# Performance work log

Hardware: AMD Instinct MI355X
Metric: run time of the kernel (lower is better)

## Reference

```python
import jax, jax.numpy as jnp
import numpy as np

N, NF, D, GH, E, B = 4096, 128, 64, 64, 32768, 32
NG, STEPS = 3, 3  # n_gcn, set2set processing steps


def setup_inputs() -> dict:
    key = jax.random.key(0)
    ks = iter(jax.random.split(key, 64))
    nrm = lambda shape: jax.random.normal(next(ks), shape, dtype=jnp.float32) * 0.05
    inp = {
        'x': jax.random.normal(next(ks), (N, NF), dtype=jnp.float32),
        'edge_attr': jax.random.uniform(next(ks), (E,), dtype=jnp.float32),
        'edge_idx': jax.random.randint(next(ks), (2, E), 0, N),
        'batch_map': jnp.sort(jax.random.randint(next(ks), (N,), 0, B)),
        # pre-GC MLP: NF->D, D->D, D->D (ReLU each)
        'pre_W0': nrm((NF, D)), 'pre_b0': nrm((D,)),
        'pre_W1': nrm((D, D)), 'pre_b1': nrm((D,)),
        'pre_W2': nrm((D, D)), 'pre_b2': nrm((D,)),
        # NNConv edge nets (stacked over NG layers): 1->GH->D*D
        'enn_W1': nrm((NG, 1, GH)), 'enn_b1': nrm((NG, GH)),
        'enn_W2': nrm((NG, GH, D * D)), 'enn_b2': nrm((NG, D * D)),
        'root_W': nrm((NG, D, D)), 'conv_b': nrm((NG, D)),
        # GRU(D, D) per layer, gate order r,z,n (torch), stored transposed for x@W
        'gru_Wih': nrm((NG, D, 3 * D)), 'gru_Whh': nrm((NG, D, 3 * D)),
        'gru_bih': nrm((NG, 3 * D)), 'gru_bhh': nrm((NG, 3 * D)),
        # Set2Set LSTM: input 2D -> hidden D, gate order i,f,g,o (torch)
        's2s_Wih': nrm((2 * D, 4 * D)), 's2s_Whh': nrm((D, 4 * D)),
        's2s_bih': nrm((4 * D,)), 's2s_bhh': nrm((4 * D,)),
        # post-GC MLP: 2D->D, D->D, D->D (ReLU each), then D->1
        'post_W0': nrm((2 * D, D)), 'post_b0': nrm((D,)),
        'post_W1': nrm((D, D)), 'post_b1': nrm((D,)),
        'post_W2': nrm((D, D)), 'post_b2': nrm((D,)),
        'post_W3': nrm((D, 1)), 'post_b3': nrm((1,)),
    }
    return inp


def _forward(x, edge_attr, pre_W0, pre_b0, pre_W1, pre_b1, pre_W2, pre_b2,
             enn_W1, enn_b1, enn_W2, enn_b2, root_W, conv_b,
             gru_Wih, gru_Whh, gru_bih, gru_bhh,
             s2s_Wih, s2s_Whh, s2s_bih, s2s_bhh,
             post_W0, post_b0, post_W1, post_b1, post_W2, post_b2,
             post_W3, post_b3, edge_idx, batch_map):
    relu, sig = jax.nn.relu, jax.nn.sigmoid
    # pre-GC layers
    out = relu(x @ pre_W0 + pre_b0)
    out = relu(out @ pre_W1 + pre_b1)
    out = relu(out @ pre_W2 + pre_b2)  # [N, D]

    src, dst = edge_idx[0], edge_idx[1]
    deg = jax.ops.segment_sum(jnp.ones((E,), out.dtype), dst, num_segments=N)
    deg = jnp.maximum(deg, 1.0)
    ea = edge_attr[:, None]  # view(-1, 1)

    for l in range(NG):
        h = out
        # NNConv: per-edge weight matrix from edge MLP
        We = relu(ea @ enn_W1[l] + enn_b1[l])              # [E, GH]
        We = (We @ enn_W2[l] + enn_b2[l]).reshape(E, D, D)  # [E, D, D]
        msg = jnp.einsum('ei,eio->eo', out[src], We)        # [E, D]
        agg = jax.ops.segment_sum(msg, dst, num_segments=N) / deg[:, None]
        conv = relu(agg + out @ root_W[l] + conv_b[l])
        # single-step GRU update (torch gate order r, z, n)
        gi = conv @ gru_Wih[l] + gru_bih[l]
        gh = h @ gru_Whh[l] + gru_bhh[l]
        i_r, i_z, i_n = jnp.split(gi, 3, axis=-1)
        h_r, h_z, h_n = jnp.split(gh, 3, axis=-1)
        r = sig(i_r + h_r)
        z = sig(i_z + h_z)
        n = jnp.tanh(i_n + r * h_n)
        out = (1.0 - z) * n + z * h

    # Set2Set pooling (early)
    q_star = jnp.zeros((B, 2 * D), out.dtype)
    hh = jnp.zeros((B, D), out.dtype)
    cc = jnp.zeros((B, D), out.dtype)
    for _ in range(STEPS):
        gates = q_star @ s2s_Wih + s2s_bih + hh @ s2s_Whh + s2s_bhh
        gi_, gf, gg, go = jnp.split(gates, 4, axis=-1)
        cc = sig(gf) * cc + sig(gi_) * jnp.tanh(gg)
        hh = sig(go) * jnp.tanh(cc)
        q = hh
        e = jnp.sum(out * q[batch_map], axis=-1)                    # [N]
        m = jax.ops.segment_max(e, batch_map, num_segments=B)
        a = jnp.exp(e - m[batch_map])
        den = jax.ops.segment_sum(a, batch_map, num_segments=B)
        a = a / den[batch_map]
        r_read = jax.ops.segment_sum(a[:, None] * out, batch_map, num_segments=B)
        q_star = jnp.concatenate([q, r_read], axis=-1)              # [B, 2D]

    # post-GC layers
    y = relu(q_star @ post_W0 + post_b0)
    y = relu(y @ post_W1 + post_b1)
    y = relu(y @ post_W2 + post_b2)
    y = y @ post_W3 + post_b3  # [B, 1]
    return y


def reference(x, edge_attr, edge_idx, batch_map, pre_W0, pre_b0, pre_W1, pre_b1,
              pre_W2, pre_b2, enn_W1, enn_b1, enn_W2, enn_b2, root_W, conv_b,
              gru_Wih, gru_Whh, gru_bih, gru_bhh, s2s_Wih, s2s_Whh, s2s_bih,
              s2s_bhh, post_W0, post_b0, post_W1, post_b1, post_W2, post_b2,
              post_W3, post_b3):
    return _forward(x, edge_attr, pre_W0, pre_b0, pre_W1, pre_b1, pre_W2, pre_b2,
                    enn_W1, enn_b1, enn_W2, enn_b2, root_W, conv_b,
                    gru_Wih, gru_Whh, gru_bih, gru_bhh,
                    s2s_Wih, s2s_Whh, s2s_bih, s2s_bhh,
                    post_W0, post_b0, post_W1, post_b1, post_W2, post_b2,
                    post_W3, post_b3, edge_idx, batch_map)
```

## Files before the change

### kernel.cpp

```cpp
#include <hip/hip_runtime.h>
#include <hip/hip_bf16.h>
#include <string.h>

#define NN   4096
#define NE   32768
#define NB   32
#define BKT  64
#define MSG_CHUNK 8

typedef __attribute__((ext_vector_type(8))) short short8;
typedef __attribute__((ext_vector_type(4))) float f4;

__device__ __forceinline__ float sigf(float x) { return 1.0f / (1.0f + __expf(-x)); }
__device__ __forceinline__ short f2bf(float f) {
    __hip_bfloat16 h = __float2bfloat16(f);
    short s;
    memcpy(&s, &h, sizeof(short));
    return s;
}

__global__ __launch_bounds__(256) void k_setup(const float* __restrict__ x,
        const float* __restrict__ W0, const float* __restrict__ b0,
        const float* __restrict__ W1, const float* __restrict__ b1,
        const float* __restrict__ W2, const float* __restrict__ b2,
        const float* __restrict__ enn_W2, __hip_bfloat16* __restrict__ W2F,
        float* __restrict__ out, float* __restrict__ agg,
        int* cnt_src, int* cnt_dst, int* bstart, int* bend) {
    int bid = blockIdx.x, t = threadIdx.x;
    if (bid < 32) {
        int i = bid * 256 + t;
        if (i < NN) cnt_src[i] = 0;
        else cnt_dst[i - NN] = 0;
        if (i < NB) { bstart[i] = 0x7FFFFFFF; bend[i] = 0; }
    } else if (bid < 224) {
        __shared__ __hip_bfloat16 tile[4096];
        size_t base = (size_t)(bid - 32) * 4096;
        for (int i = t; i < 4096; i += 256) {
            int k = i >> 6, o = i & 63;
            int pos = ((o >> 4) << 10) | ((k >> 5) << 9) | (((k >> 3) & 3) << 7)
                    | ((o & 15) << 3) | (k & 7);
            tile[pos] = __float2bfloat16(enn_W2[base + i]);
        }
        __syncthreads();
        for (int i = t; i < 4096; i += 256) W2F[base + i] = tile[i];
    } else {
        __shared__ float xr[4][128], ha[4][64], hb[4][64];
        int w = t >> 6, j = t & 63;
        int n = (bid - 224) * 4 + w;
        xr[w][j] = x[(size_t)n * 128 + j];
        xr[w][64 + j] = x[(size_t)n * 128 + 64 + j];
        agg[(size_t)n * 64 + j] = 0.f;
        float s = b0[j];
        #pragma unroll 8
        for (int k = 0; k < 128; ++k) s = fmaf(xr[w][k], W0[k * 64 + j], s);
        ha[w][j] = fmaxf(s, 0.f);
        s = b1[j];
        #pragma unroll 8
        for (int k = 0; k < 64; ++k) s = fmaf(ha[w][k], W1[k * 64 + j], s);
        hb[w][j] = fmaxf(s, 0.f);
        s = b2[j];
        #pragma unroll 8
        for (int k = 0; k < 64; ++k) s = fmaf(hb[w][k], W2[k * 64 + j], s);
        out[(size_t)n * 64 + j] = fmaxf(s, 0.f);
    }
}

__global__ __launch_bounds__(256) void k_bucket(const int* __restrict__ eidx,
        const float* __restrict__ ea, const int* __restrict__ bm,
        int* cnt_src, int* cnt_dst, int* csr_dst, float* csr_ea,
        int* bstart, int* bend) {
    int e = blockIdx.x * 256 + threadIdx.x;
    if (e < NE) {
        int s = eidx[e];
        int d = eidx[NE + e];
        int slot = atomicAdd(&cnt_src[s], 1);
        if (slot < BKT) {
            csr_dst[s * BKT + slot] = d;
            csr_ea[s * BKT + slot] = ea[e];
        }
        atomicAdd(&cnt_dst[d], 1);
    }
    if (e < NN) {
        int b = bm[e];
        atomicMin(&bstart[b], e);
        atomicMax(&bend[b], e + 1);
    }
}

__global__ __launch_bounds__(256, 2) void k_fused(const float* __restrict__ out,
        const __hip_bfloat16* __restrict__ W2F_l, const float* __restrict__ b2l,
        const float* __restrict__ W1l, const float* __restrict__ b1l,
        const int* __restrict__ cnt_src, const int* __restrict__ csr_dst,
        const float* __restrict__ csr_ea, float* __restrict__ agg) {
    __shared__ __hip_bfloat16 Pt[8 * 4096];
    __shared__ float outs[8][68];
    __shared__ float wlds[4][MSG_CHUNK][64];
    int t = threadIdx.x, wave = t >> 6, lane = t & 63;
    int laneM = lane & 15, quad = lane >> 4;
    int n0 = blockIdx.x * 8;
    for (int i = t; i < 512; i += 256) outs[i >> 6][i & 63] = out[(size_t)n0 * 64 + i];
    __syncthreads();
    short8 a0, a1;
    {
        const float* ar = &outs[laneM & 7][quad * 8];
        #pragma unroll
        for (int j = 0; j < 8; ++j) a0[j] = f2bf(ar[j]);
        const float* ar2 = &outs[laneM & 7][32 + quad * 8];
        #pragma unroll
        for (int j = 0; j < 8; ++j) a1[j] = f2bf(ar2[j]);
    }
    float btr[2] = {0.f, 0.f};
    for (int k = 0; k < 64; ++k) {
        float bv = b2l[k * 64 + lane];
        #pragma unroll
        for (int u = 0; u < 2; ++u) btr[u] = fmaf(outs[wave * 2 + u][k], bv, btr[u]);
    }
    #pragma unroll 2
    for (int gp = 0; gp < 8; ++gp) {
        int gA = wave * 16 + gp * 2;
        const __hip_bfloat16* BgA = W2F_l + (size_t)gA * 4096;
        const __hip_bfloat16* BgB = BgA + 4096;
        int c = gA >> 3;
        int p = (gA >> 1) & 3;
        char* wb = (char*)Pt + (quad << 15) + (c << 10) + (laneM << 4)
                 + (((p ^ quad) & 3) << 2);
        #pragma unroll
        for (int sub = 0; sub < 4; ++sub) {
            short8 bA0 = *(const short8*)(BgA + sub * 1024 + lane * 8);
            short8 bA1 = *(const short8*)(BgA + sub * 1024 + 512 + lane * 8);
            short8 bB0 = *(const short8*)(BgB + sub * 1024 + lane * 8);
            short8 bB1 = *(const short8*)(BgB + sub * 1024 + 512 + lane * 8);
            f4 accA = {0.f, 0.f, 0.f, 0.f}, accB = {0.f, 0.f, 0.f, 0.f};
            accA = __builtin_amdgcn_mfma_f32_16x16x32_bf16(a0, bA0, accA, 0, 0, 0);
            accA = __builtin_amdgcn_mfma_f32_16x16x32_bf16(a1, bA1, accA, 0, 0, 0);
            accB = __builtin_amdgcn_mfma_f32_16x16x32_bf16(a0, bB0, accB, 0, 0, 0);
            accB = __builtin_amdgcn_mfma_f32_16x16x32_bf16(a1, bB1, accB, 0, 0, 0);
            if (quad < 2) {
                char* wbs = wb + (sub << 8);
                #pragma unroll
                for (int r = 0; r < 4; ++r) {
                    unsigned pk = (unsigned)(unsigned short)f2bf(accA[r])
                                | ((unsigned)(unsigned short)f2bf(accB[r]) << 16);
                    *(unsigned*)(wbs + (r << 13)) = pk;
                }
            }
        }
    }
    __syncthreads();
    float w1v = W1l[lane], b1v = b1l[lane];
    for (int u = 0; u < 2; ++u) {
        int nloc = wave * 2 + u;
        int n = n0 + nloc;
        int deg = cnt_src[n];
        if (deg > BKT) deg = BKT;
        if (deg <= 0) continue;
        int wq = nloc >> 2;
        float preg[64];
        const char* Pn = (const char*)Pt + (nloc << 13);
        #pragma unroll
        for (int c = 0; c < 8; ++c) {
            uint4 vv = *(const uint4*)(Pn + (c << 10) + (lane << 4));
            unsigned d0 = vv.x, d1 = vv.y, d2 = vv.z, d3 = vv.w;
            if (wq & 1) { unsigned tt = d0; d0 = d1; d1 = tt; tt = d2; d2 = d3; d3 = tt; }
            union { unsigned u2; float f; } cv;
            cv.u2 = d0 << 16;          preg[c * 8 + 0] = cv.f;
            cv.u2 = d0 & 0xFFFF0000u;  preg[c * 8 + 1] = cv.f;
            cv.u2 = d1 << 16;          preg[c * 8 + 2] = cv.f;
            cv.u2 = d1 & 0xFFFF0000u;  preg[c * 8 + 3] = cv.f;
            cv.u2 = d2 << 16;          preg[c * 8 + 4] = cv.f;
            cv.u2 = d2 & 0xFFFF0000u;  preg[c * 8 + 5] = cv.f;
            cv.u2 = d3 << 16;          preg[c * 8 + 6] = cv.f;
            cv.u2 = d3 & 0xFFFF0000u;  preg[c * 8 + 7] = cv.f;
        }
        float bt = btr[u];
        const int* bdst = csr_dst + n * BKT;
        const float* bea = csr_ea + n * BKT;
        for (int c0 = 0; c0 < deg; c0 += MSG_CHUNK) {
            int cc = deg - c0;
            if (cc > MSG_CHUNK) cc = MSG_CHUNK;
            int dl = 0; float el = 0.f;
            if (lane < cc) { dl = bdst[c0 + lane]; el = bea[c0 + lane]; }
            for (int si = 0; si < cc; ++si) {
                float eav = __shfl(el, si, 64);
                wlds[wave][si][lane] = fmaxf(fmaf(eav, w1v, b1v), 0.f);
            }
            for (int i = 0; i < cc; ++i) {
                int dst = __shfl(dl, i, 64);
                const float* wr = wlds[wave][i];
                float acc0 = bt, acc1 = 0.f, acc2 = 0.f, acc3 = 0.f;
                #pragma unroll
                for (int g = 0; g < 64; g += 16) {
                    float4 w0 = *(const float4*)(wr + g);
                    float4 w1 = *(const float4*)(wr + g + 4);
                    float4 w2 = *(const float4*)(wr + g + 8);
                    float4 w3 = *(const float4*)(wr + g + 12);
                    acc0 = fmaf(w0.x, preg[g], acc0);
                    acc0 = fmaf(w0.y, preg[g + 1], acc0);
                    acc0 = fmaf(w0.z, preg[g + 2], acc0);
                    acc0 = fmaf(w0.w, preg[g + 3], acc0);
                    acc1 = fmaf(w1.x, preg[g + 4], acc1);
                    acc1 = fmaf(w1.y, preg[g + 5], acc1);
                    acc1 = fmaf(w1.z, preg[g + 6], acc1);
                    acc1 = fmaf(w1.w, preg[g + 7], acc1);
                    acc2 = fmaf(w2.x, preg[g + 8], acc2);
                    acc2 = fmaf(w2.y, preg[g + 9], acc2);
                    acc2 = fmaf(w2.z, preg[g + 10], acc2);
                    acc2 = fmaf(w2.w, preg[g + 11], acc2);
                    acc3 = fmaf(w3.x, preg[g + 12], acc3);
                    acc3 = fmaf(w3.y, preg[g + 13], acc3);
                    acc3 = fmaf(w3.z, preg[g + 14], acc3);
                    acc3 = fmaf(w3.w, preg[g + 15], acc3);
                }
                float acc = (acc0 + acc1) + (acc2 + acc3);
                atomicAdd(&agg[(size_t)dst * 64 + lane], acc);
            }
        }
    }
}

__global__ __launch_bounds__(256) void k_gru(const float* __restrict__ out,
        float* __restrict__ agg, const int* __restrict__ cnt_dst,
        const float* __restrict__ rootW, const float* __restrict__ convb,
        const float* __restrict__ Wih, const float* __restrict__ Whh,
        const float* __restrict__ bih, const float* __restrict__ bhh,
        float* __restrict__ outn) {
    __shared__ float sh[4][64], sc[4][64];
    int t = threadIdx.x, w = t >> 6, j = t & 63;
    int n = blockIdx.x * 4 + w;
    float hj = out[(size_t)n * 64 + j];
    sh[w][j] = hj;
    int dg = cnt_dst[n];
    float invd = 1.0f / (float)(dg > 0 ? dg : 1);
    float av = agg[(size_t)n * 64 + j];
    agg[(size_t)n * 64 + j] = 0.f;
    __syncthreads();
    float s = av * invd + convb[j];
    #pragma unroll 8
    for (int k = 0; k < 64; ++k) s = fmaf(sh[w][k], rootW[k * 64 + j], s);
    float conv = fmaxf(s, 0.f);
    sc[w][j] = conv;
    __syncthreads();
    float gir = bih[j], giz = bih[64 + j], gin = bih[128 + j];
    float ghr = bhh[j], ghz = bhh[64 + j], ghn = bhh[128 + j];
    #pragma unroll 4
    for (int k = 0; k < 64; ++k) {
        float c = sc[w][k], h = sh[w][k];
        gir = fmaf(c, Wih[k * 192 + j], gir);
        giz = fmaf(c, Wih[k * 192 + 64 + j], giz);
        gin = fmaf(c, Wih[k * 192 + 128 + j], gin);
        ghr = fmaf(h, Whh[k * 192 + j], ghr);
        ghz = fmaf(h, Whh[k * 192 + 64 + j], ghz);
        ghn = fmaf(h, Whh[k * 192 + 128 + j], ghn);
    }
    float r = sigf(gir + ghr);
    float z = sigf(giz + ghz);
    float nn = tanhf(gin + r * ghn);
    outn[(size_t)n * 64 + j] = (1.f - z) * nn + z * hj;
}

__global__ __launch_bounds__(1024) void k_s2s_post(const float* __restrict__ out,
        const int* __restrict__ bstart, const int* __restrict__ bend,
        const float* __restrict__ Wih, const float* __restrict__ Whh,
        const float* __restrict__ bih, const float* __restrict__ bhh,
        const float* __restrict__ pW0, const float* __restrict__ pb0,
        const float* __restrict__ pW1, const float* __restrict__ pb1,
        const float* __restrict__ pW2, const float* __restrict__ pb2,
        const float* __restrict__ pW3, const float* __restrict__ pb3,
        float* __restrict__ y) {
    __shared__ float cache[192 * 65];
    __shared__ float qs[128], hh[64], cc[64], gates[256];
    __shared__ float ebuf[1024];
    __shared__ float redbuf[1024];
    __shared__ float redw[16];
    __shared__ float smax, sinv;
    __shared__ float tmp64[64];
    int t = threadIdx.x, wave = t >> 6, lane = t & 63;
    int b = blockIdx.x;
    int s0 = bstart[b], e0 = bend[b];
    int cnt = e0 - s0;
    if (cnt < 0) cnt = 0;
    if (cnt > 1024) cnt = 1024;
    int ccnt = cnt < 192 ? cnt : 192;
    for (int li = t; li < ccnt * 64; li += 1024) {
        int rowi = li >> 6, d = li & 63;
        cache[rowi * 65 + d] = out[(size_t)(s0 + rowi) * 64 + d];
    }
    int g = t & 255, seg = t >> 8;
    const float* wp;
    int kcnt;
    if (seg == 0)      { wp = Wih + g;             kcnt = 64; }
    else if (seg == 1) { wp = Wih + 64 * 256 + g;  kcnt = 64; }
    else if (seg == 2) { wp = Whh + g;             kcnt = 32; }
    else               { wp = Whh + 32 * 256 + g;  kcnt = 32; }
    float wreg[64];
    #pragma unroll
    for (int j = 0; j < 64; ++j)
        wreg[j] = (j < kcnt) ? wp[(size_t)j * 256] : 0.f;
    if (t < 128) qs[t] = 0.f;
    if (t < 64) { hh[t] = 0.f; cc[t] = 0.f; }
    __syncthreads();
    for (int step = 0; step < 3; ++step) {
        const float* vsrc = (seg == 0) ? qs : (seg == 1) ? qs + 64
                          : (seg == 2) ? hh : hh + 32;
        float partial = 0.f;
        #pragma unroll
        for (int j = 0; j < 64; ++j)
            if (j < kcnt) partial = fmaf(vsrc[j], wreg[j], partial);
        redbuf[seg * 256 + g] = partial;
        __syncthreads();
        if (t < 256)
            gates[t] = bih[t] + bhh[t] + redbuf[t] + redbuf[256 + t]
                     + redbuf[512 + t] + redbuf[768 + t];
        __syncthreads();
        if (t < 64) {
            float cn = sigf(gates[64 + t]) * cc[t] + sigf(gates[t]) * tanhf(gates[128 + t]);
            cc[t] = cn;
            hh[t] = sigf(gates[192 + t]) * tanhf(cn);
        }
        __syncthreads();
        for (int idx = t; idx < cnt; idx += 1024) {
            float s = 0.f;
            if (idx < 192) {
                const float* row = cache + idx * 65;
                #pragma unroll 8
                for (int d = 0; d < 64; ++d) s = fmaf(row[d], hh[d], s);
            } else {
                const float* row = out + (size_t)(s0 + idx) * 64;
                for (int d = 0; d < 64; ++d) s = fmaf(row[d], hh[d], s);
            }
            ebuf[idx] = s;
        }
        __syncthreads();
        float lm = (t < cnt) ? ebuf[t] : -3.0e38f;
        #pragma unroll
        for (int off = 32; off > 0; off >>= 1) lm = fmaxf(lm, __shfl_down(lm, off, 64));
        if (lane == 0) redw[wave] = lm;
        __syncthreads();
        if (t == 0) {
            float m = redw[0];
            #pragma unroll
            for (int w2 = 1; w2 < 16; ++w2) m = fmaxf(m, redw[w2]);
            smax = m;
        }
        __syncthreads();
        float m = smax;
        float av = 0.f;
        if (t < cnt) {
            av = __expf(ebuf[t] - m);
            ebuf[t] = av;
        }
        float ls = av;
        #pragma unroll
        for (int off = 32; off > 0; off >>= 1) ls += __shfl_down(ls, off, 64);
        if (lane == 0) redw[wave] = ls;
        __syncthreads();
        if (t == 0) {
            float s = 0.f;
            #pragma unroll
            for (int w2 = 0; w2 < 16; ++w2) s += redw[w2];
            sinv = (cnt > 0) ? 1.f / s : 0.f;
        }
        __syncthreads();
        float inv = sinv;
        float r = 0.f;
        for (int idx = wave; idx < cnt; idx += 16) {
            float a = ebuf[idx];
            float v = (idx < 192) ? cache[idx * 65 + lane]
                                  : out[(size_t)(s0 + idx) * 64 + lane];
            r = fmaf(a, v, r);
        }
        redbuf[wave * 64 + lane] = r;
        __syncthreads();
        if (t < 64) {
            float s = 0.f;
            #pragma unroll
            for (int w2 = 0; w2 < 16; ++w2) s += redbuf[w2 * 64 + t];
            qs[64 + t] = s * inv;
            qs[t] = hh[t];
        }
        __syncthreads();
    }
    if (t < 64) {
        float s = pb0[t];
        #pragma unroll 4
        for (int k = 0; k < 128; ++k) s = fmaf(qs[k], pW0[k * 64 + t], s);
        tmp64[t] = fmaxf(s, 0.f);
    }
    __syncthreads();
    float h1v = 0.f;
    if (t < 64) {
        float s = pb1[t];
        #pragma unroll 4
        for (int k = 0; k < 64; ++k) s = fmaf(tmp64[k], pW1[k * 64 + t], s);
        h1v = fmaxf(s, 0.f);
    }
    __syncthreads();
    if (t < 64) tmp64[t] = h1v;
    __syncthreads();
    if (t < 64) {
        float s = pb2[t];
        #pragma unroll 4
        for (int k = 0; k < 64; ++k) s = fmaf(tmp64[k], pW2[k * 64 + t], s);
        gates[t] = fmaxf(s, 0.f) * pW3[t];
    }
    __syncthreads();
    if (t == 0) {
        float yy = pb3[0];
        for (int k = 0; k < 64; ++k) yy += gates[k];
        y[b] = yy;
    }
}


extern "C" void kernel_launch(void* const* d_in, const int* in_sizes, int n_in,
                              void* d_out, int out_size, void* d_ws, size_t ws_size,
                              hipStream_t stream) {
    const float* x         = (const float*)d_in[0];
    const float* edge_attr = (const float*)d_in[1];
    const int*   edge_idx  = (const int*)d_in[2];
    const int*   batch_map = (const int*)d_in[3];
    const float* pre_W0 = (const float*)d_in[4];
    const float* pre_b0 = (const float*)d_in[5];
    const float* pre_W1 = (const float*)d_in[6];
    const float* pre_b1 = (const float*)d_in[7];
    const float* pre_W2 = (const float*)d_in[8];
    const float* pre_b2 = (const float*)d_in[9];
    const float* enn_W1 = (const float*)d_in[10];
    const float* enn_b1 = (const float*)d_in[11];
    const float* enn_W2 = (const float*)d_in[12];
    const float* enn_b2 = (const float*)d_in[13];
    const float* root_W = (const float*)d_in[14];
    const float* conv_b = (const float*)d_in[15];
    const float* gru_Wih = (const float*)d_in[16];
    const float* gru_Whh = (const float*)d_in[17];
    const float* gru_bih = (const float*)d_in[18];
    const float* gru_bhh = (const float*)d_in[19];
    const float* s2s_Wih = (const float*)d_in[20];
    const float* s2s_Whh = (const float*)d_in[21];
    const float* s2s_bih = (const float*)d_in[22];
    const float* s2s_bhh = (const float*)d_in[23];
    const float* post_W0 = (const float*)d_in[24];
    const float* post_b0 = (const float*)d_in[25];
    const float* post_W1 = (const float*)d_in[26];
    const float* post_b1 = (const float*)d_in[27];
    const float* post_W2 = (const float*)d_in[28];
    const float* post_b2 = (const float*)d_in[29];
    const float* post_W3 = (const float*)d_in[30];
    const float* post_b3 = (const float*)d_in[31];
    float* yout = (float*)d_out;

    char* wp = (char*)d_ws;
    auto take = [&](size_t bytes) -> char* {
        char* r = wp;
        wp += (bytes + 255) & ~(size_t)255;
        return r;
    };
    float* outA = (float*)take((size_t)NN * 64 * 4);
    float* outB = (float*)take((size_t)NN * 64 * 4);
    float* agg  = (float*)take((size_t)NN * 64 * 4);
    __hip_bfloat16* W2F = (__hip_bfloat16*)take((size_t)3 * 64 * 4096 * 2);
    int* cnt_src  = (int*)take((size_t)NN * 4);
    int* cnt_dst  = (int*)take((size_t)NN * 4);
    int* csr_dst  = (int*)take((size_t)NN * BKT * 4);
    float* csr_ea = (float*)take((size_t)NN * BKT * 4);
    int* bstart   = (int*)take((size_t)NB * 4);
    int* bend     = (int*)take((size_t)NB * 4);

    k_setup<<<1248, 256, 0, stream>>>(x, pre_W0, pre_b0, pre_W1, pre_b1, pre_W2, pre_b2,
                                      enn_W2, W2F, outA, agg, cnt_src, cnt_dst,
                                      bstart, bend);
    k_bucket<<<128, 256, 0, stream>>>(edge_idx, edge_attr, batch_map, cnt_src, cnt_dst,
                                      csr_dst, csr_ea, bstart, bend);

    float* cur = outA;
    float* nxt = outB;
    for (int l = 0; l < 3; ++l) {
        k_fused<<<NN / 8, 256, 0, stream>>>(cur, W2F + (size_t)l * 64 * 4096,
                                            enn_b2 + (size_t)l * 4096,
                                            enn_W1 + l * 64, enn_b1 + l * 64,
                                            cnt_src, csr_dst, csr_ea, agg);
        k_gru<<<NN / 4, 256, 0, stream>>>(cur, agg, cnt_dst, root_W + l * 4096,
                                          conv_b + l * 64, gru_Wih + l * 64 * 192,
                                          gru_Whh + l * 64 * 192, gru_bih + l * 192,
                                          gru_bhh + l * 192, nxt);
        float* tmp = cur; cur = nxt; nxt = tmp;
    }
    k_s2s_post<<<NB, 1024, 0, stream>>>(cur, bstart, bend, s2s_Wih, s2s_Whh, s2s_bih,
                                        s2s_bhh, post_W0, post_b0, post_W1, post_b1,
                                        post_W2, post_b2, post_W3, post_b3, yout);
}
```

Baseline: 353.1 us.

## Restructure Set2Set kernel to 256 threads with full per-thread gate weights

The Set2Set+post-MLP kernel drops from 1024 to 256 threads per block. Each thread now holds a full column of the LSTM input and hidden weights (192 registers), so the cross-segment reduction buffer goes away. The node cache is stored transposed, the softmax reductions use xor shuffles with fewer barriers, and the inner loops use four independent accumulators. This cuts synchronisation and shared-memory traffic in a latency-bound kernel, but each thread now carries much higher register pressure and does more serial work.

Result: no change. 359.2 us (+1.7%).

```diff
diff --git a/kernel.cpp b/kernel.cpp
--- a/kernel.cpp
+++ b/kernel.cpp
@@ -258,7 +258,7 @@
     outn[(size_t)n * 64 + j] = (1.f - z) * nn + z * hj;
 }
 
-__global__ __launch_bounds__(1024) void k_s2s_post(const float* __restrict__ out,
+__global__ __launch_bounds__(256, 1) void k_s2s_post(const float* __restrict__ out,
         const int* __restrict__ bstart, const int* __restrict__ bend,
         const float* __restrict__ Wih, const float* __restrict__ Whh,
         const float* __restrict__ bih, const float* __restrict__ bhh,
@@ -267,12 +267,13 @@
         const float* __restrict__ pW2, const float* __restrict__ pb2,
         const float* __restrict__ pW3, const float* __restrict__ pb3,
         float* __restrict__ y) {
-    __shared__ float cache[192 * 65];
-    __shared__ float qs[128], hh[64], cc[64], gates[256];
+    __shared__ float cacheT[64 * 193];
+    __shared__ float qs[128];
+    __shared__ float hh_l[64];
+    __shared__ float gates_l[256];
     __shared__ float ebuf[1024];
-    __shared__ float redbuf[1024];
-    __shared__ float redw[16];
-    __shared__ float smax, sinv;
+    __shared__ float redw[4], redw2[4];
+    __shared__ float redbuf[4][64];
     __shared__ float tmp64[64];
     int t = threadIdx.x, wave = t >> 6, lane = t & 63;
     int b = blockIdx.x;
@@ -281,102 +282,104 @@
     if (cnt < 0) cnt = 0;
     if (cnt > 1024) cnt = 1024;
     int ccnt = cnt < 192 ? cnt : 192;
-    for (int li = t; li < ccnt * 64; li += 1024) {
-        int rowi = li >> 6, d = li & 63;
-        cache[rowi * 65 + d] = out[(size_t)(s0 + rowi) * 64 + d];
-    }
-    int g = t & 255, seg = t >> 8;
-    const float* wp;
-    int kcnt;
-    if (seg == 0)      { wp = Wih + g;             kcnt = 64; }
-    else if (seg == 1) { wp = Wih + 64 * 256 + g;  kcnt = 64; }
-    else if (seg == 2) { wp = Whh + g;             kcnt = 32; }
-    else               { wp = Whh + 32 * 256 + g;  kcnt = 32; }
-    float wreg[64];
+    for (int i = t; i < ccnt * 64; i += 256) {
+        int row = i >> 6, d = i & 63;
+        cacheT[d * 193 + row] = out[(size_t)(s0 + row) * 64 + d];
+    }
+    float wih[128], whh[64];
     #pragma unroll
-    for (int j = 0; j < 64; ++j)
-        wreg[j] = (j < kcnt) ? wp[(size_t)j * 256] : 0.f;
+    for (int j = 0; j < 128; ++j) wih[j] = Wih[(size_t)j * 256 + t];
+    #pragma unroll
+    for (int j = 0; j < 64; ++j) whh[j] = Whh[(size_t)j * 256 + t];
+    float bsum = bih[t] + bhh[t];
+    float ccr = 0.f;
     if (t < 128) qs[t] = 0.f;
-    if (t < 64) { hh[t] = 0.f; cc[t] = 0.f; }
-    __syncthreads();
+    if (t < 64) hh_l[t] = 0.f;
+    __syncthreads();
+    const float4* qs4 = (const float4*)qs;
+    const float4* hh4 = (const float4*)hh_l;
     for (int step = 0; step < 3; ++step) {
-        const float* vsrc = (seg == 0) ? qs : (seg == 1) ? qs + 64
-                          : (seg == 2) ? hh : hh + 32;
-        float partial = 0.f;
-        #pragma unroll
-        for (int j = 0; j < 64; ++j)
-            if (j < kcnt) partial = fmaf(vsrc[j], wreg[j], partial);
-        redbuf[seg * 256 + g] = partial;
-        __syncthreads();
-        if (t < 256)
-            gates[t] = bih[t] + bhh[t] + redbuf[t] + redbuf[256 + t]
-                     + redbuf[512 + t] + redbuf[768 + t];
+        float g0 = bsum, g1 = 0.f, g2 = 0.f, g3 = 0.f;
+        #pragma unroll
+        for (int jq = 0; jq < 32; ++jq) {
+            float4 v = qs4[jq];
+            g0 = fmaf(v.x, wih[jq * 4 + 0], g0);
+            g1 = fmaf(v.y, wih[jq * 4 + 1], g1);
+            g2 = fmaf(v.z, wih[jq * 4 + 2], g2);
+            g3 = fmaf(v.w, wih[jq * 4 + 3], g3);
+        }
+        #pragma unroll
+        for (int jq = 0; jq < 16; ++jq) {
+            float4 v = hh4[jq];
+            g0 = fmaf(v.x, whh[jq * 4 + 0], g0);
+            g1 = fmaf(v.y, whh[jq * 4 + 1], g1);
+            g2 = fmaf(v.z, whh[jq * 4 + 2], g2);
+            g3 = fmaf(v.w, whh[jq * 4 + 3], g3);
+        }
+        gates_l[t] = (g0 + g1) + (g2 + g3);
         __syncthreads();
         if (t < 64) {
-            float cn = sigf(gates[64 + t]) * cc[t] + sigf(gates[t]) * tanhf(gates[128 + t]);
-            cc[t] = cn;
-            hh[t] = sigf(gates[192 + t]) * tanhf(cn);
-        }
-        __syncthreads();
-        for (int idx = t; idx < cnt; idx += 1024) {
-            float s = 0.f;
+            float cn = sigf(gates_l[64 + t]) * ccr
+                     + sigf(gates_l[t]) * tanhf(gates_l[128 + t]);
+            ccr = cn;
+            hh_l[t] = sigf(gates_l[192 + t]) * tanhf(cn);
+        }
+        __syncthreads();
+        for (int idx = t; idx < cnt; idx += 256) {
+            float s0a = 0.f, s1a = 0.f, s2a = 0.f, s3a = 0.f;
             if (idx < 192) {
-                const float* row = cache + idx * 65;
-                #pragma unroll 8
-                for (int d = 0; d < 64; ++d) s = fmaf(row[d], hh[d], s);
+                #pragma unroll
+                for (int dq = 0; dq < 16; ++dq) {
+                    float4 h = hh4[dq];
+                    s0a = fmaf(cacheT[(dq * 4 + 0) * 193 + idx], h.x, s0a);
+                    s1a = fmaf(cacheT[(dq * 4 + 1) * 193 + idx], h.y, s1a);
+                    s2a = fmaf(cacheT[(dq * 4 + 2) * 193 + idx], h.z, s2a);
+                    s3a = fmaf(cacheT[(dq * 4 + 3) * 193 + idx], h.w, s3a);
+                }
             } else {
                 const float* row = out + (size_t)(s0 + idx) * 64;
-                for (int d = 0; d < 64; ++d) s = fmaf(row[d], hh[d], s);
+                #pragma unroll
+                for (int dq = 0; dq < 16; ++dq) {
+                    float4 h = hh4[dq];
+                    s0a = fmaf(row[dq * 4 + 0], h.x, s0a);
+                    s1a = fmaf(row[dq * 4 + 1], h.y, s1a);
+                    s2a = fmaf(row[dq * 4 + 2], h.z, s2a);
+                    s3a = fmaf(row[dq * 4 + 3], h.w, s3a);
+                }
             }
-            ebuf[idx] = s;
-        }
-        __syncthreads();
-        float lm = (t < cnt) ? ebuf[t] : -3.0e38f;
-        #pragma unroll
-        for (int off = 32; off > 0; off >>= 1) lm = fmaxf(lm, __shfl_down(lm, off, 64));
+            ebuf[idx] = (s0a + s1a) + (s2a + s3a);
+        }
+        __syncthreads();
+        float lm = -3.0e38f;
+        for (int idx = t; idx < cnt; idx += 256) lm = fmaxf(lm, ebuf[idx]);
+        #pragma unroll
+        for (int off = 32; off > 0; off >>= 1) lm = fmaxf(lm, __shfl_xor(lm, off, 64));
         if (lane == 0) redw[wave] = lm;
         __syncthreads();
-        if (t == 0) {
-            float m = redw[0];
-            #pragma unroll
-            for (int w2 = 1; w2 < 16; ++w2) m = fmaxf(m, redw[w2]);
-            smax = m;
-        }
-        __syncthreads();
-        float m = smax;
-        float av = 0.f;
-        if (t < cnt) {
-            av = __expf(ebuf[t] - m);
-            ebuf[t] = av;
-        }
-        float ls = av;
-        #pragma unroll
-        for (int off = 32; off > 0; off >>= 1) ls += __shfl_down(ls, off, 64);
-        if (lane == 0) redw[wave] = ls;
-        __syncthreads();
-        if (t == 0) {
-            float s = 0.f;
-            #pragma unroll
-            for (int w2 = 0; w2 < 16; ++w2) s += redw[w2];
-            sinv = (cnt > 0) ? 1.f / s : 0.f;
-        }
-        __syncthreads();
-        float inv = sinv;
-        float r = 0.f;
-        for (int idx = wave; idx < cnt; idx += 16) {
-            float a = ebuf[idx];
-            float v = (idx < 192) ? cache[idx * 65 + lane]
-                                  : out[(size_t)(s0 + idx) * 64 + lane];
-            r = fmaf(a, v, r);
-        }
-        redbuf[wave * 64 + lane] = r;
+        float m = fmaxf(fmaxf(redw[0], redw[1]), fmaxf(redw[2], redw[3]));
+        float ls = 0.f;
+        for (int idx = t; idx < cnt; idx += 256) {
+            float a = __expf(ebuf[idx] - m);
+            ebuf[idx] = a;
+            ls += a;
+        }
+        #pragma unroll
+        for (int off = 32; off > 0; off >>= 1) ls += __shfl_xor(ls, off, 64);
+        if (lane == 0) redw2[wave] = ls;
+        __syncthreads();
+        float ssum = (redw2[0] + redw2[1]) + (redw2[2] + redw2[3]);
+        float inv = (cnt > 0) ? 1.f / ssum : 0.f;
+        float r0 = 0.f;
+        for (int row = wave; row < ccnt; row += 4)
+            r0 = fmaf(ebuf[row], cacheT[lane * 193 + row], r0);
+        for (int row = 192 + wave; row < cnt; row += 4)
+            r0 = fmaf(ebuf[row], out[(size_t)(s0 + row) * 64 + lane], r0);
+        redbuf[wave][lane] = r0;
         __syncthreads();
         if (t < 64) {
-            float s = 0.f;
-            #pragma unroll
-            for (int w2 = 0; w2 < 16; ++w2) s += redbuf[w2 * 64 + t];
+            float s = ((redbuf[0][t] + redbuf[1][t]) + (redbuf[2][t] + redbuf[3][t]));
             qs[64 + t] = s * inv;
-            qs[t] = hh[t];
+            qs[t] = hh_l[t];
         }
         __syncthreads();
     }
@@ -401,12 +404,12 @@
         float s = pb2[t];
         #pragma unroll 4
         for (int k = 0; k < 64; ++k) s = fmaf(tmp64[k], pW2[k * 64 + t], s);
-        gates[t] = fmaxf(s, 0.f) * pW3[t];
+        gates_l[t] = fmaxf(s, 0.f) * pW3[t];
     }
     __syncthreads();
     if (t == 0) {
         float yy = pb3[0];
-        for (int k = 0; k < 64; ++k) yy += gates[k];
+        for (int k = 0; k < 64; ++k) yy += gates_l[k];
         y[b] = yy;
     }
 }
@@ -485,7 +488,7 @@
                                           gru_bhh + l * 192, nxt);
         float* tmp = cur; cur = nxt; nxt = tmp;
     }
-    k_s2s_post<<<NB, 1024, 0, stream>>>(cur, bstart, bend, s2s_Wih, s2s_Whh, s2s_bih,
-                                        s2s_bhh, post_W0, post_b0, post_W1, post_b1,
-                                        post_W2, post_b2, post_W3, post_b3, yout);
-}
+    k_s2s_post<<<NB, 256, 0, stream>>>(cur, bstart, bend, s2s_Wih, s2s_Whh, s2s_bih,
+                                       s2s_bhh, post_W0, post_b0, post_W1, post_b1,
+                                       post_W2, post_b2, post_W3, post_b3, yout);
+}
```
